# Kernel optimization log

Hardware: AMD Instinct MI355X
Metric: run time of the kernel (lower is better)

The kernel has to match this reference:

```python
import jax, jax.numpy as jnp
import numpy as np

NUM_CLASSES = 8      # cls-head channels per anchor; channel 0 = background
A = 3                # anchors per location (aspect ratios 0.5, 1.0, 2.0)
K = 500              # fixed pre-NMS top-k per (image, class, level)
SCORE_TH = 0.05
IOU_TH = 0.5
# (H, W, stride, anchor_size) per FPN level for a 1536x1536 image
LEVELS = ((192, 192, 8, 16.0), (96, 96, 16, 32.0), (48, 48, 32, 64.0))
ARS = np.array([0.5, 1.0, 2.0], dtype=np.float32)


def make_anchors(H, W, stride, size):
    w = size * np.sqrt(ARS)           # (A,)
    h = size / np.sqrt(ARS)
    cx = (np.arange(W, dtype=np.float32) + 0.5) * stride
    cy = (np.arange(H, dtype=np.float32) + 0.5) * stride
    cy, cx = np.meshgrid(cy, cx, indexing='ij')   # (H, W)
    x1 = cx[..., None] - 0.5 * w
    y1 = cy[..., None] - 0.5 * h
    x2 = cx[..., None] + 0.5 * w
    y2 = cy[..., None] + 0.5 * h
    return jnp.asarray(np.stack([x1, y1, x2, y2], -1).reshape(-1, 4))  # (H*W*A, 4)


def decode(anchors, deltas):
    # anchors (N,4) xyxy, deltas (B,N,4) -> boxes (B,N,4); matches source decode math
    wa = anchors[:, 2] - anchors[:, 0]
    ha = anchors[:, 3] - anchors[:, 1]
    cxa = anchors[:, 0] + 0.5 * wa
    cya = anchors[:, 1] + 0.5 * ha
    dx, dy, dw, dh = deltas[..., 0], deltas[..., 1], deltas[..., 2], deltas[..., 3]
    cx = dx * wa + cxa
    cy = dy * ha + cya
    w = jnp.exp(dw) * wa
    h = jnp.exp(dh) * ha
    return jnp.stack([cx - 0.5 * w, cy - 0.5 * h, cx + 0.5 * w, cy + 0.5 * h], -1)


def nms_one(boxes, scores):
    # boxes (N,4), scores (N,) for one (image, class). Fixed-shape exact greedy NMS
    # over the top-K candidates (boxes below SCORE_TH are invalidated, matching the
    # source's mask; K bounds the candidate set for jit-compatibility).
    sc, idx = jax.lax.top_k(scores, K)
    b = boxes[idx]                                        # (K,4) sorted by score desc
    valid = sc > SCORE_TH
    area = (b[:, 2] - b[:, 0]) * (b[:, 3] - b[:, 1])
    ix1 = jnp.maximum(b[:, None, 0], b[None, :, 0])
    iy1 = jnp.maximum(b[:, None, 1], b[None, :, 1])
    ix2 = jnp.minimum(b[:, None, 2], b[None, :, 2])
    iy2 = jnp.minimum(b[:, None, 3], b[None, :, 3])
    inter = jnp.maximum(ix2 - ix1, 0.0) * jnp.maximum(iy2 - iy1, 0.0)
    union = area[:, None] + area[None, :] - inter
    iou = inter / jnp.maximum(union, 1e-9)                # (K,K)
    r = jnp.arange(K)

    def body(i, keep):
        sup = (iou[i] > IOU_TH) & (r > i) & keep[i]
        return keep & ~sup

    keep = jax.lax.fori_loop(0, K, body, valid)
    return b, sc, keep


def level_postprocess(cls_p, reg_p, anchors):
    B = cls_p.shape[0]
    # (B, A*C, H, W) -> sigmoid scores (B, N, C); (B, A*4, H, W) -> deltas (B, N, 4)
    scores = jax.nn.sigmoid(cls_p.transpose(0, 2, 3, 1).reshape(B, -1, NUM_CLASSES))
    deltas = reg_p.transpose(0, 2, 3, 1).reshape(B, -1, 4)
    boxes = decode(anchors, deltas)                       # (B, N, 4)
    fg = scores[:, :, 1:]                                 # foreground classes 1..C-1

    def per_image(b_i, s_i):                              # b_i (N,4), s_i (N, C-1)
        return jax.vmap(lambda s: nms_one(b_i, s))(s_i.T)

    return jax.vmap(per_image)(boxes, fg)                 # each (B, C-1, K, ...)


def setup_inputs() -> dict:
    key = jax.random.key(0)
    ks = jax.random.split(key, 6)
    B = 16
    inp = {}
    for i, (H, W, _, _) in enumerate(LEVELS):
        # cls logits shifted by -4 ~ RetinaNet prior bias so only a sparse subset
        # passes the 0.05 threshold; reg deltas small-scale like trained outputs.
        inp[f'cls_p{i + 3}'] = jax.random.normal(ks[i], (B, A * NUM_CLASSES, H, W), jnp.float32) - 4.0
        inp[f'reg_p{i + 3}'] = jax.random.normal(ks[i + 3], (B, A * 4, H, W), jnp.float32) * 0.1
    return inp


def reference(cls_p3, cls_p4, cls_p5, reg_p3, reg_p4, reg_p5):
    cls_ps = (cls_p3, cls_p4, cls_p5)
    reg_ps = (reg_p3, reg_p4, reg_p5)
    boxes_l, scores_l, keep_l = [], [], []
    for cls_p, reg_p, (H, W, stride, size) in zip(cls_ps, reg_ps, LEVELS):
        anchors = make_anchors(H, W, stride, size)
        b, s, k = level_postprocess(cls_p, reg_p, anchors)
        boxes_l.append(b)
        scores_l.append(s)
        keep_l.append(k)
    boxes = jnp.stack(boxes_l)      # (3, B, C-1, K, 4)
    scores = jnp.stack(scores_l)    # (3, B, C-1, K)
    keep = jnp.stack(keep_l)        # (3, B, C-1, K) bool
    B = cls_p3.shape[0]
    labels = jnp.broadcast_to(jnp.arange(NUM_CLASSES - 1)[None, None, :, None],
                              (3, B, NUM_CLASSES - 1, K))
    return boxes, scores, keep, labels
```

## Files before the change

kernel.cpp:

```cpp
#include <hip/hip_runtime.h>
#include <stdint.h>


namespace {
constexpr int KSEL = 500;
constexpr int CAP  = 1024;
constexpr int BIMG = 16;
constexpr int NCLS = 7;
constexpr int NPROB = 336;
constexpr int OFF_SCORES = 672000;
constexpr int OFF_KEEP   = 840000;
constexpr int OFF_LABELS = 1008000;

constexpr unsigned KEY_F0 = 2051;
constexpr unsigned KEY_F1 = 2045;
constexpr unsigned KEY_F2 = 2039;

constexpr unsigned SB15 = (0x3D000000u >> 15);
constexpr int NB15 = 2048;

constexpr int NB_SCAN = 1232;
constexpr int SEG0 = 384;
constexpr int SEG1 = 1024;
constexpr int SEG2 = 1536;
constexpr size_t L1_POOL_BASE = (size_t)896 * SEG0;
constexpr size_t L2_POOL_BASE = L1_POOL_BASE + (size_t)224 * SEG1;
constexpr size_t POOL_ENTRIES = L2_POOL_BASE + (size_t)112 * SEG2;

constexpr size_t CCNT_OFF   = 0;
constexpr size_t CHIST_OFF  = 8192;
constexpr size_t CHIST_BYTES = (size_t)NB_SCAN * NB15 * 4;
constexpr size_t POOL_OFF   = CHIST_OFF + CHIST_BYTES;
constexpr size_t POOL_BYTES = POOL_ENTRIES * 8;
constexpr size_t WS_NEED    = POOL_OFF + POOL_BYTES;

__constant__ unsigned char c_tb[36] = {
    0,0,0,0,0,0,0,0, 1,1,1,1,1,1,1, 2,2,2,2,2,2,
    3,3,3,3,3, 4,4,4,4, 5,5,5, 6,6, 7};
__constant__ unsigned char c_tw[36] = {
    0,1,2,3,4,5,6,7, 1,2,3,4,5,6,7, 2,3,4,5,6,7,
    3,4,5,6,7, 4,5,6,7, 5,6,7, 6,7, 7};

typedef float f4v __attribute__((ext_vector_type(4)));
}

__device__ __forceinline__ float sigmoid_ref(float x) {
#pragma clang fp contract(off)
    return 1.0f / (1.0f + expf(-x));
}

__device__ __forceinline__ unsigned mono_key(float x) {
    unsigned b = __float_as_uint(x);
    unsigned m = (b & 0x80000000u) ? 0xFFFFFFFFu : 0x80000000u;
    return b ^ m;
}

__device__ __forceinline__ void scan_decode(int bx, int& l, int& img, int& c,
                                            int& p, int& HW, int& hw0, int& hw1) {
    int pidL, chunk, chunkHW;
    if (bx < 896)        { l = 0; pidL = bx >> 3;         chunk = bx & 7;         chunkHW = 4608; HW = 36864; }
    else if (bx < 1120)  { l = 1; pidL = (bx - 896) >> 1; chunk = (bx - 896) & 1; chunkHW = 4608; HW = 9216; }
    else                 { l = 2; pidL = bx - 1120;       chunk = 0;              chunkHW = 2304; HW = 2304; }
    img = pidL / NCLS; c = pidL % NCLS;
    p = (l * BIMG + img) * NCLS + c;
    hw0 = chunk * chunkHW; hw1 = hw0 + chunkHW;
}

__global__ __launch_bounds__(256) void k_scan(
    const float* __restrict__ cls0, const float* __restrict__ cls1,
    const float* __restrict__ cls2, unsigned* __restrict__ g_ccnt,
    unsigned long long* __restrict__ g_pool, unsigned* __restrict__ g_chist)
{
    const int tid = threadIdx.x;
    int l, img, c, p, HW, hw0, hw1;
    scan_decode(blockIdx.x, l, img, c, p, HW, hw0, hw1);
    (void)p;
    const float* cls = (l == 0) ? cls0 : (l == 1) ? cls1 : cls2;
    const unsigned keyf = (l == 0) ? KEY_F0 : (l == 1) ? KEY_F1 : KEY_F2;
    const int segCap = (l == 0) ? SEG0 : (l == 1) ? SEG1 : SEG2;
    size_t segOff;
    if (l == 0)      segOff = (size_t)blockIdx.x * SEG0;
    else if (l == 1) segOff = L1_POOL_BASE + (size_t)(blockIdx.x - 896) * SEG1;
    else             segOff = L2_POOL_BASE + (size_t)(blockIdx.x - 1120) * SEG2;

    __shared__ unsigned long long buf[SEG2];
    __shared__ unsigned lh[NB15];
    __shared__ int s_n;
    for (int i = tid; i < NB15; i += 256) lh[i] = 0u;
    if (tid == 0) s_n = 0;
    __syncthreads();

    const int n4 = (hw1 - hw0) >> 2;
    for (int a = 0; a < 3; ++a) {
        const f4v* pb4 = (const f4v*)(cls
            + (size_t)(img * 24 + a * 8 + c + 1) * (size_t)HW + (size_t)hw0);
        for (int idx = tid; idx < n4; idx += 256) {
            f4v v = __builtin_nontemporal_load(pb4 + idx);
            float mx = fmaxf(fmaxf(v.x, v.y), fmaxf(v.z, v.w));
            if ((mono_key(mx) >> 19) < keyf) continue;
            const int hwb = hw0 + idx * 4;
            float vv[4] = {v.x, v.y, v.z, v.w};
#pragma unroll
            for (int q = 0; q < 4; ++q) {
                if ((mono_key(vv[q]) >> 19) >= keyf) {
                    int pos = atomicAdd(&s_n, 1);
                    unsigned bits = __float_as_uint(sigmoid_ref(vv[q]));
                    unsigned bin = (bits >> 15) - SB15;
                    if (bin > (unsigned)(NB15 - 1)) bin = NB15 - 1;
                    atomicAdd(&lh[bin], 1u);
                    if (pos < segCap) {
                        unsigned n = (unsigned)((hwb + q) * 3 + a);
                        buf[pos] = ((unsigned long long)bits << 32)
                                 | (unsigned long long)(0xFFFFFFFFu - n);
                    }
                }
            }
        }
    }
    __syncthreads();
    int m = s_n; if (m > segCap) m = segCap;
    unsigned long long* seg = g_pool + segOff;
    for (int i = tid; i < m; i += 256) seg[i] = buf[i];
    unsigned* ch = g_chist + (size_t)blockIdx.x * NB15;
    for (int i = tid; i < NB15; i += 256) ch[i] = lh[i];
    if (tid == 0) g_ccnt[blockIdx.x] = (unsigned)m;
}

__global__ __launch_bounds__(512) void k_nms2(
    const float* __restrict__ reg0, const float* __restrict__ reg1,
    const float* __restrict__ reg2, const unsigned* __restrict__ g_ccnt,
    const unsigned long long* __restrict__ g_pool,
    const unsigned* __restrict__ g_chist, float* __restrict__ out)
{
    const int p    = blockIdx.x;
    const int l    = p / (BIMG * NCLS);
    const int rem  = p % (BIMG * NCLS);
    const int bimg = rem / NCLS;
    const int c    = rem % NCLS;
    const int tid  = threadIdx.x;
    const int lane = tid & 63;
    const int wid  = tid >> 6;

    int W, HW; float stride, asize;
    const float* reg;
    int nseg, segEnt, ccntBase;
    size_t segOff0;
    if (l == 0)      { W = 192; HW = 36864; stride = 8.0f;  asize = 16.0f; reg = reg0;
                       nseg = 8; segEnt = SEG0; ccntBase = rem * 8;
                       segOff0 = (size_t)rem * 8 * SEG0; }
    else if (l == 1) { W = 96;  HW = 9216;  stride = 16.0f; asize = 32.0f; reg = reg1;
                       nseg = 2; segEnt = SEG1; ccntBase = 896 + rem * 2;
                       segOff0 = L1_POOL_BASE + (size_t)rem * 2 * SEG1; }
    else             { W = 48;  HW = 2304;  stride = 32.0f; asize = 64.0f; reg = reg2;
                       nseg = 1; segEnt = SEG2; ccntBase = 1120 + rem;
                       segOff0 = L2_POOL_BASE + (size_t)rem * SEG2; }

    __shared__ union {
        struct { unsigned h[NB15]; unsigned s4[512]; } a;
        struct { float4 box4[512]; float sarea[512]; } b;
    } u;
    __shared__ unsigned sup[64];
    __shared__ unsigned s_t;
    __shared__ int      s_n;
    __shared__ unsigned long long s_keys[CAP];
    __shared__ unsigned long long s_sorted[CAP];
    __shared__ unsigned long long s_mask[8][512];
    __shared__ unsigned long long s_alive[8];

    for (int i = tid; i < NB15; i += 512) {
        unsigned acc = 0;
        for (int s = 0; s < nseg; ++s)
            acc += g_chist[(size_t)(ccntBase + s) * NB15 + i];
        u.a.h[i] = acc;
    }
    for (int i = tid; i < CAP; i += 512) s_sorted[i] = 0ull;
    if (tid == 0) { s_t = 0u; s_n = 0; }
    __syncthreads();

    {
        unsigned cs = u.a.h[tid * 4] + u.a.h[tid * 4 + 1]
                    + u.a.h[tid * 4 + 2] + u.a.h[tid * 4 + 3];
        u.a.s4[tid] = cs;
    }
    __syncthreads();
    if (tid < 64) {
        unsigned ss = 0;
#pragma unroll
        for (int k = 0; k < 8; ++k) ss += u.a.s4[tid * 8 + k];
        sup[tid] = ss;
    }
    __syncthreads();
    if (tid < 64) {
        unsigned Sab = 0;
        for (int j = tid + 1; j < 64; ++j) Sab += sup[j];
        if (Sab < (unsigned)KSEL && Sab + sup[tid] >= (unsigned)KSEL) {
            unsigned acc = Sab;
            int t = tid * 32;
            for (int b = tid * 32 + 31; b >= tid * 32; --b) {
                acc += u.a.h[b];
                if (acc >= (unsigned)KSEL) { t = b; break; }
            }
            s_t = (unsigned)t;
        }
    }
    __syncthreads();

    const unsigned t  = s_t;
    const unsigned tg = (t > 0u) ? (t - 1u) : 0u;
    const unsigned cut = (tg + SB15) << 15;

    for (int s = 0; s < nseg; ++s) {
        const unsigned long long* seg = g_pool + segOff0 + (size_t)s * segEnt;
        unsigned cn = g_ccnt[ccntBase + s]; if (cn > (unsigned)segEnt) cn = segEnt;
        for (int i = tid; i < (int)cn; i += 512) {
            unsigned long long key = seg[i];
            if ((unsigned)(key >> 32) >= cut) {
                int pos = atomicAdd(&s_n, 1);
                if (pos < CAP) s_keys[pos] = key;
            }
        }
    }
    __syncthreads();
    const int mm = (s_n > CAP) ? CAP : s_n;

    for (int i = tid; i < mm; i += 512) {
        const unsigned long long ki = s_keys[i];
        int rank = 0;
        for (int j = 0; j < mm; ++j) rank += (int)(s_keys[j] > ki);
        if (rank < CAP) s_sorted[rank] = ki;
    }
    __syncthreads();

    float4* outBoxes4 = (float4*)(out + (size_t)p * (size_t)(KSEL * 4));
    float* outScores = out + OFF_SCORES + (size_t)p * KSEL;
    float* outLabels = out + OFF_LABELS + (size_t)p * KSEL;

    {
        const int r = tid;
        bool pred = false;
        if (r < KSEL) {
            unsigned long long key = s_sorted[r];
            unsigned bits = (unsigned)(key >> 32);
            float sc = __uint_as_float(bits);
            unsigned n = 0xFFFFFFFFu - (unsigned)(key & 0xFFFFFFFFull);
            int a  = (int)(n % 3u);
            int hw = (int)(n / 3u);
            int h2 = hw / W, w = hw % W;
            float b0, b1, b2, b3;
            {
#pragma clang fp contract(off)
                float ar  = (a == 0) ? 0.5f : ((a == 1) ? 1.0f : 2.0f);
                float sq  = sqrtf(ar);
                float was = asize * sq;
                float has = asize / sq;
                float cx0 = ((float)w + 0.5f) * stride;
                float cy0 = ((float)h2 + 0.5f) * stride;
                float x1 = cx0 - 0.5f * was;
                float y1 = cy0 - 0.5f * has;
                float x2 = cx0 + 0.5f * was;
                float y2 = cy0 + 0.5f * has;
                float wa = x2 - x1;
                float ha = y2 - y1;
                float cxa = x1 + 0.5f * wa;
                float cya = y1 + 0.5f * ha;
                const float* rp = reg + (size_t)(bimg * 12 + a * 4) * (size_t)HW + (size_t)hw;
                float dx = rp[0];
                float dy = rp[(size_t)HW];
                float dw = rp[(size_t)2 * HW];
                float dh = rp[(size_t)3 * HW];
                float bcx = dx * wa + cxa;
                float bcy = dy * ha + cya;
                float bw  = expf(dw) * wa;
                float bh  = expf(dh) * ha;
                b0 = bcx - 0.5f * bw;
                b1 = bcy - 0.5f * bh;
                b2 = bcx + 0.5f * bw;
                b3 = bcy + 0.5f * bh;
                u.b.box4[r]  = make_float4(b0, b1, b2, b3);
                u.b.sarea[r] = (b2 - b0) * (b3 - b1);
            }
            outBoxes4[r] = make_float4(b0, b1, b2, b3);
            outScores[r] = sc;
            outLabels[r] = (float)c;
            pred = sc > 0.05f;
        }
        unsigned long long bal = __ballot((int)pred);
        if (lane == 0) s_alive[wid] = bal;
    }
    __syncthreads();

    for (int t2 = wid; t2 < 36; t2 += 8) {
        const int b = (int)c_tb[t2];
        const int w = (int)c_tw[t2];
        const int r2 = b * 64 + lane;
        const float4 rb = u.b.box4[r2];
        const float  A0 = u.b.sarea[r2];
        const int jn = (w * 64 + 64 <= KSEL) ? 64 : (KSEL - w * 64);
        const unsigned long long full =
            (jn == 64) ? ~0ull : ((1ull << jn) - 1ull);

        unsigned long long m = 0ull;
#pragma unroll
        for (int k = 0; k < 64; ++k) {
#pragma clang fp contract(off)
            float4 cb = u.b.box4[w * 64 + k];
            float  ja = u.b.sarea[w * 64 + k];
            float ix1 = fmaxf(rb.x, cb.x);
            float iy1 = fmaxf(rb.y, cb.y);
            float ix2 = fminf(rb.z, cb.z);
            float iy2 = fminf(rb.w, cb.w);
            float iw = fmaxf(ix2 - ix1, 0.0f);
            float ih = fmaxf(iy2 - iy1, 0.0f);
            float inter = iw * ih;
            float uni = A0 + ja - inter;
            float uc  = fmaxf(uni, 1e-9f);
            if (inter + inter > uc) m |= (1ull << k);
        }
        m &= full;
        if (b == w) m &= ~(1ull << lane);

        s_mask[w][r2] = m;
    }
    __syncthreads();

    if (wid == 0) {
        unsigned long long alive[8];
#pragma unroll
        for (int w = 0; w < 8; ++w) alive[w] = s_alive[w];

#pragma unroll
        for (int b = 0; b < 8; ++b) {
            unsigned long long a64 = alive[b];
            if (!a64) continue;
            const unsigned long long diag = s_mask[b][b * 64 + lane];
            const unsigned long long hiL =
                (lane < 63) ? (~0ull << (lane + 1)) : 0ull;

            unsigned long long work = a64, removed = 0ull;
            while (true) {
                bool active = (((work >> lane) & 1ull) != 0ull) &&
                              ((diag & work & hiL) != 0ull);
                unsigned long long act = __ballot((int)active);
                if (!act) break;
                int j = __ffsll((long long)act) - 1;
                unsigned long long wj = __ballot((int)((diag >> j) & 1ull));
                unsigned long long hij = (j < 63) ? (~0ull << (j + 1)) : 0ull;
                wj &= hij;
                removed |= wj;
                work &= hij;
                work &= ~wj;
            }
            const unsigned long long kept = a64 & ~removed;
            alive[b] = kept;

            if (b < 7 && kept) {
                const bool iskept = ((kept >> lane) & 1ull) != 0ull;
#pragma unroll
                for (int w = b + 1; w < 8; ++w) {
                    unsigned long long v = s_mask[w][b * 64 + lane];
                    unsigned long long contrib = iskept ? v : 0ull;
                    if (!__any((int)(contrib != 0ull))) continue;
#pragma unroll
                    for (int s = 32; s >= 1; s >>= 1)
                        contrib |= __shfl_xor(contrib, s);
                    alive[w] &= ~contrib;
                }
            }
        }

        float* outKeep = out + OFF_KEEP + (size_t)p * KSEL;
#pragma unroll
        for (int it = 0; it < 8; ++it) {
            int r = it * 64 + lane;
            if (r < KSEL)
                outKeep[r] = ((alive[r >> 6] >> (r & 63)) & 1ull) ? 1.0f : 0.0f;
        }
    }
}

__global__ __launch_bounds__(256) void retina_post_kernel(
    const float* __restrict__ cls0, const float* __restrict__ reg0,
    const float* __restrict__ cls1, const float* __restrict__ reg1,
    const float* __restrict__ cls2, const float* __restrict__ reg2,
    float* __restrict__ out)
{
    const int bx   = blockIdx.x;
    const int l    = bx / (BIMG * NCLS);
    const int rem  = bx % (BIMG * NCLS);
    const int bimg = rem / NCLS;
    const int c    = rem % NCLS;
    const int tid  = threadIdx.x;
    const int lane = tid & 63;
    const int wid  = tid >> 6;

    int H, W; float stride, asize;
    const float *cls, *reg;
    if (l == 0)      { H = 192; W = 192; stride = 8.0f;  asize = 16.0f; cls = cls0; reg = reg0; }
    else if (l == 1) { H = 96;  W = 96;  stride = 16.0f; asize = 32.0f; cls = cls1; reg = reg1; }
    else             { H = 48;  W = 48;  stride = 32.0f; asize = 64.0f; cls = cls2; reg = reg2; }
    const int HW = H * W;
    const int c1 = c + 1;

    __shared__ unsigned long long s_keys[CAP];
    __shared__ float              s_box[KSEL * 4];
    __shared__ float              s_area[KSEL];
    __shared__ unsigned long long s_mask[KSEL * 8];
    __shared__ unsigned long long s_alive[8];
    __shared__ unsigned           s_hist[4 * 16];
    __shared__ unsigned           s_prefix;
    __shared__ unsigned           s_cgt;
    __shared__ int                s_m;
    __shared__ int                s_need4;
    __shared__ int                s_gshift;

    for (int i = tid; i < CAP; i += 256) s_keys[i] = 0ull;
    if (tid == 0) { s_prefix = 0u; s_cgt = 0u; s_m = 0; s_need4 = 0; s_gshift = 20; }

    for (int pass = 0; pass < 4; ++pass) {
        if (pass == 3 && !s_need4) break;
        if (tid < 64) s_hist[tid] = 0u;
        __syncthreads();
        const unsigned pref = s_prefix;
        const unsigned cgt  = s_cgt;
        const int shp = 32 - 4 * pass;
        const int shn = 28 - 4 * pass;
        unsigned cnt[16];
#pragma unroll
        for (int q = 0; q < 16; ++q) cnt[q] = 0u;
        for (int a = 0; a < 3; ++a) {
            const float* p = cls + (size_t)(bimg * 24 + a * 8 + c1) * (size_t)HW;
            for (int hw = tid; hw < HW; hw += 256) {
                float s = sigmoid_ref(p[hw]);
                unsigned bits = __float_as_uint(s);
                bool match = (pass == 0) || ((bits >> shp) == pref);
                unsigned sel = match ? ((bits >> shn) & 0xFu) : 0xFFu;
#pragma unroll
                for (int q = 0; q < 16; ++q) {
                    unsigned long long bal = __ballot((int)(sel == (unsigned)q));
                    cnt[q] += (unsigned)__popcll(bal);
                }
            }
        }
        if (lane == 0) {
#pragma unroll
            for (int q = 0; q < 16; ++q) s_hist[wid * 16 + q] = cnt[q];
        }
        __syncthreads();
        if (tid == 0) {
            unsigned tot[16];
#pragma unroll
            for (int q = 0; q < 16; ++q)
                tot[q] = s_hist[q] + s_hist[16 + q] + s_hist[32 + q] + s_hist[48 + q];
            unsigned acc = cgt;
            int t = 0;
            for (int q = 15; q >= 0; --q) {
                if (acc + tot[q] >= (unsigned)KSEL) { t = q; break; }
                acc += tot[q];
            }
            s_prefix = (pref << 4) | (unsigned)t;
            s_cgt = acc;
            if (pass == 2) s_need4 = (acc + tot[t] > (unsigned)CAP) ? 1 : 0;
            if (pass == 3) s_gshift = 16;
        }
        __syncthreads();
    }

    {
        const unsigned gpref = s_prefix;
        const int gsh = s_gshift;
        for (int a = 0; a < 3; ++a) {
            const float* p = cls + (size_t)(bimg * 24 + a * 8 + c1) * (size_t)HW;
            for (int hw = tid; hw < HW; hw += 256) {
                float s = sigmoid_ref(p[hw]);
                unsigned bits = __float_as_uint(s);
                if ((bits >> gsh) >= gpref) {
                    int pos = atomicAdd(&s_m, 1);
                    if (pos < CAP) {
                        unsigned n = (unsigned)(hw * 3 + a);
                        s_keys[pos] = ((unsigned long long)bits << 32)
                                    | (unsigned long long)(0xFFFFFFFFu - n);
                    }
                }
            }
        }
    }

    for (int k2 = 2; k2 <= CAP; k2 <<= 1) {
        for (int j = k2 >> 1; j >= 1; j >>= 1) {
            __syncthreads();
            for (int i = tid; i < CAP; i += 256) {
                int ixj = i ^ j;
                if (ixj > i) {
                    unsigned long long va = s_keys[i], vb = s_keys[ixj];
                    bool desc = ((i & k2) == 0);
                    if (desc ? (va < vb) : (va > vb)) {
                        s_keys[i] = vb; s_keys[ixj] = va;
                    }
                }
            }
        }
    }
    __syncthreads();

    const size_t probIdx  = (size_t)((l * BIMG + bimg) * NCLS + c);
    float* outBoxes  = out + probIdx * (size_t)(KSEL * 4);
    float* outScores = out + OFF_SCORES + probIdx * (size_t)KSEL;
    float* outKeep   = out + OFF_KEEP   + probIdx * (size_t)KSEL;
    float* outLabels = out + OFF_LABELS + probIdx * (size_t)KSEL;

    for (int it = 0; it < 2; ++it) {
        int r = it * 256 + tid;
        bool pred = false;
        if (r < KSEL) {
            unsigned long long key = s_keys[r];
            unsigned bits = (unsigned)(key >> 32);
            float sc = __uint_as_float(bits);
            unsigned n = 0xFFFFFFFFu - (unsigned)(key & 0xFFFFFFFFull);
            int a  = (int)(n % 3u);
            int hw = (int)(n / 3u);
            int h = hw / W, w = hw % W;
            float b0, b1, b2, b3;
            {
#pragma clang fp contract(off)
                float ar  = (a == 0) ? 0.5f : ((a == 1) ? 1.0f : 2.0f);
                float sq  = sqrtf(ar);
                float was = asize * sq;
                float has = asize / sq;
                float cx0 = ((float)w + 0.5f) * stride;
                float cy0 = ((float)h + 0.5f) * stride;
                float x1 = cx0 - 0.5f * was;
                float y1 = cy0 - 0.5f * has;
                float x2 = cx0 + 0.5f * was;
                float y2 = cy0 + 0.5f * has;
                float wa = x2 - x1;
                float ha = y2 - y1;
                float cxa = x1 + 0.5f * wa;
                float cya = y1 + 0.5f * ha;
                const float* rp = reg + (size_t)(bimg * 12 + a * 4) * (size_t)HW + (size_t)hw;
                float dx = rp[0];
                float dy = rp[(size_t)HW];
                float dw = rp[(size_t)2 * HW];
                float dh = rp[(size_t)3 * HW];
                float bcx = dx * wa + cxa;
                float bcy = dy * ha + cya;
                float bw  = expf(dw) * wa;
                float bh  = expf(dh) * ha;
                b0 = bcx - 0.5f * bw;
                b1 = bcy - 0.5f * bh;
                b2 = bcx + 0.5f * bw;
                b3 = bcy + 0.5f * bh;
                s_box[r * 4 + 0] = b0; s_box[r * 4 + 1] = b1;
                s_box[r * 4 + 2] = b2; s_box[r * 4 + 3] = b3;
                s_area[r] = (b2 - b0) * (b3 - b1);
            }
            outBoxes[r * 4 + 0] = b0; outBoxes[r * 4 + 1] = b1;
            outBoxes[r * 4 + 2] = b2; outBoxes[r * 4 + 3] = b3;
            outScores[r] = sc;
            outLabels[r] = (float)c;
            pred = sc > 0.05f;
        }
        unsigned long long bal = __ballot((int)pred);
        if (lane == 0) s_alive[it * 4 + wid] = bal;
    }
    __syncthreads();

    for (int i = tid; i < KSEL; i += 256) {
        float x1i = s_box[i * 4 + 0], y1i = s_box[i * 4 + 1];
        float x2i = s_box[i * 4 + 2], y2i = s_box[i * 4 + 3];
        float ai = s_area[i];
        for (int ww = 0; ww < 8; ++ww) {
            unsigned long long m = 0ull;
            int jbase = ww * 64;
            int jend = jbase + 64; if (jend > KSEL) jend = KSEL;
            int j0 = jbase > (i + 1) ? jbase : (i + 1);
            for (int j = j0; j < jend; ++j) {
#pragma clang fp contract(off)
                float ix1 = fmaxf(x1i, s_box[j * 4 + 0]);
                float iy1 = fmaxf(y1i, s_box[j * 4 + 1]);
                float ix2 = fminf(x2i, s_box[j * 4 + 2]);
                float iy2 = fminf(y2i, s_box[j * 4 + 3]);
                float iw = fmaxf(ix2 - ix1, 0.0f);
                float ih = fmaxf(iy2 - iy1, 0.0f);
                float inter = iw * ih;
                float uni = ai + s_area[j] - inter;
                float iou = inter / fmaxf(uni, 1e-9f);
                if (iou > 0.5f) m |= (1ull << (j - jbase));
            }
            s_mask[i * 8 + ww] = m;
        }
    }
    __syncthreads();

    if (tid < 64) {
        unsigned long long al = (lane < 8) ? s_alive[lane] : 0ull;
        for (int i = 0; i < KSEL; ++i) {
            unsigned long long aw = __shfl(al, i >> 6);
            if ((aw >> (i & 63)) & 1ull) {
                if (lane < 8) al &= ~s_mask[i * 8 + lane];
            }
        }
        if (lane < 8) s_alive[lane] = al;
    }
    __syncthreads();

    for (int it = 0; it < 2; ++it) {
        int r = it * 256 + tid;
        if (r < KSEL) {
            unsigned long long w64 = s_alive[r >> 6];
            outKeep[r] = ((w64 >> (r & 63)) & 1ull) ? 1.0f : 0.0f;
        }
    }
}

extern "C" void kernel_launch(void* const* d_in, const int* in_sizes, int n_in,
                              void* d_out, int out_size, void* d_ws, size_t ws_size,
                              hipStream_t stream) {
    (void)out_size;
    const float *cls0 = nullptr, *reg0 = nullptr, *cls1 = nullptr,
                *reg1 = nullptr, *cls2 = nullptr, *reg2 = nullptr;
    for (int i = 0; i < n_in; ++i) {
        switch (in_sizes[i]) {
            case 14155776: cls0 = (const float*)d_in[i]; break;
            case 7077888:  reg0 = (const float*)d_in[i]; break;
            case 3538944:  cls1 = (const float*)d_in[i]; break;
            case 1769472:  reg1 = (const float*)d_in[i]; break;
            case 884736:   cls2 = (const float*)d_in[i]; break;
            case 442368:   reg2 = (const float*)d_in[i]; break;
            default: break;
        }
    }
    float* out = (float*)d_out;

    if (ws_size < WS_NEED) {
        retina_post_kernel<<<dim3(NPROB), dim3(256), 0, stream>>>(
            cls0, reg0, cls1, reg1, cls2, reg2, out);
        return;
    }

    unsigned*           g_ccnt  = (unsigned*)((char*)d_ws + CCNT_OFF);
    unsigned*           g_chist = (unsigned*)((char*)d_ws + CHIST_OFF);
    unsigned long long* g_pool  = (unsigned long long*)((char*)d_ws + POOL_OFF);

    k_scan<<<dim3(NB_SCAN), dim3(256), 0, stream>>>(cls0, cls1, cls2,
                                                    g_ccnt, g_pool, g_chist);
    k_nms2<<<dim3(NPROB), dim3(512), 0, stream>>>(reg0, reg1, reg2,
                                                  g_ccnt, g_pool, g_chist,
                                                  out);
}
```

Measured before the change: 209.0 us.

## Coarsen score histogram, fuse rank sort with box decode, readlane IoU operands

The score histogram shrinks from 2048 to 512 bins, so each NMS block accumulates and scans fewer bins and the scan kernel writes less histogram data to global memory. The separate rank-sort pass into s_sorted is removed: each thread computes its candidate's rank, issues the regression loads before the rank loop so their latency overlaps it, then writes the decoded box directly at its rank and sets alive bits with shared atomicOr. The IoU mask loop now broadcasts column boxes with readlane instead of reading them from LDS at each step. Coarser bins may pass more candidates above the cutoff, which can make the O(n^2) rank count costlier, and boxes at ranks the candidates do not fill are no longer explicitly zeroed.

```diff
diff --git a/kernel.cpp b/kernel.cpp
--- a/kernel.cpp
+++ b/kernel.cpp
@@ -16,8 +16,8 @@
 constexpr unsigned KEY_F1 = 2045;
 constexpr unsigned KEY_F2 = 2039;
 
-constexpr unsigned SB15 = (0x3D000000u >> 15);
-constexpr int NB15 = 2048;
+constexpr unsigned SBH = (0x3D000000u >> 17);
+constexpr int NBH = 512;
 
 constexpr int NB_SCAN = 1232;
 constexpr int SEG0 = 384;
@@ -29,7 +29,7 @@
 
 constexpr size_t CCNT_OFF   = 0;
 constexpr size_t CHIST_OFF  = 8192;
-constexpr size_t CHIST_BYTES = (size_t)NB_SCAN * NB15 * 4;
+constexpr size_t CHIST_BYTES = (size_t)NB_SCAN * NBH * 4;
 constexpr size_t POOL_OFF   = CHIST_OFF + CHIST_BYTES;
 constexpr size_t POOL_BYTES = POOL_ENTRIES * 8;
 constexpr size_t WS_NEED    = POOL_OFF + POOL_BYTES;
@@ -53,6 +53,10 @@
     unsigned b = __float_as_uint(x);
     unsigned m = (b & 0x80000000u) ? 0xFFFFFFFFu : 0x80000000u;
     return b ^ m;
+}
+
+__device__ __forceinline__ float rl(float v, int k) {
+    return __uint_as_float(__builtin_amdgcn_readlane(__float_as_uint(v), k));
 }
 
 __device__ __forceinline__ void scan_decode(int bx, int& l, int& img, int& c,
@@ -84,9 +88,9 @@
     else             segOff = L2_POOL_BASE + (size_t)(blockIdx.x - 1120) * SEG2;
 
     __shared__ unsigned long long buf[SEG2];
-    __shared__ unsigned lh[NB15];
+    __shared__ unsigned lh[NBH];
     __shared__ int s_n;
-    for (int i = tid; i < NB15; i += 256) lh[i] = 0u;
+    for (int i = tid; i < NBH; i += 256) lh[i] = 0u;
     if (tid == 0) s_n = 0;
     __syncthreads();
 
@@ -105,8 +109,8 @@
                 if ((mono_key(vv[q]) >> 19) >= keyf) {
                     int pos = atomicAdd(&s_n, 1);
                     unsigned bits = __float_as_uint(sigmoid_ref(vv[q]));
-                    unsigned bin = (bits >> 15) - SB15;
-                    if (bin > (unsigned)(NB15 - 1)) bin = NB15 - 1;
+                    unsigned bin = (bits >> 17) - SBH;
+                    if (bin > (unsigned)(NBH - 1)) bin = NBH - 1;
                     atomicAdd(&lh[bin], 1u);
                     if (pos < segCap) {
                         unsigned n = (unsigned)((hwb + q) * 3 + a);
@@ -121,8 +125,8 @@
     int m = s_n; if (m > segCap) m = segCap;
     unsigned long long* seg = g_pool + segOff;
     for (int i = tid; i < m; i += 256) seg[i] = buf[i];
-    unsigned* ch = g_chist + (size_t)blockIdx.x * NB15;
-    for (int i = tid; i < NB15; i += 256) ch[i] = lh[i];
+    unsigned* ch = g_chist + (size_t)blockIdx.x * NBH;
+    for (int i = tid; i < NBH; i += 256) ch[i] = lh[i];
     if (tid == 0) g_ccnt[blockIdx.x] = (unsigned)m;
 }
 
@@ -156,37 +160,30 @@
                        segOff0 = L2_POOL_BASE + (size_t)rem * SEG2; }
 
     __shared__ union {
-        struct { unsigned h[NB15]; unsigned s4[512]; } a;
+        struct { unsigned h[NBH]; } a;
         struct { float4 box4[512]; float sarea[512]; } b;
     } u;
     __shared__ unsigned sup[64];
     __shared__ unsigned s_t;
     __shared__ int      s_n;
     __shared__ unsigned long long s_keys[CAP];
-    __shared__ unsigned long long s_sorted[CAP];
     __shared__ unsigned long long s_mask[8][512];
     __shared__ unsigned long long s_alive[8];
 
-    for (int i = tid; i < NB15; i += 512) {
+    {
         unsigned acc = 0;
         for (int s = 0; s < nseg; ++s)
-            acc += g_chist[(size_t)(ccntBase + s) * NB15 + i];
-        u.a.h[i] = acc;
-    }
-    for (int i = tid; i < CAP; i += 512) s_sorted[i] = 0ull;
+            acc += g_chist[(size_t)(ccntBase + s) * NBH + tid];
+        u.a.h[tid] = acc;
+    }
+    if (tid < 8) s_alive[tid] = 0ull;
     if (tid == 0) { s_t = 0u; s_n = 0; }
     __syncthreads();
 
-    {
-        unsigned cs = u.a.h[tid * 4] + u.a.h[tid * 4 + 1]
-                    + u.a.h[tid * 4 + 2] + u.a.h[tid * 4 + 3];
-        u.a.s4[tid] = cs;
-    }
-    __syncthreads();
     if (tid < 64) {
         unsigned ss = 0;
 #pragma unroll
-        for (int k = 0; k < 8; ++k) ss += u.a.s4[tid * 8 + k];
+        for (int k = 0; k < 8; ++k) ss += u.a.h[tid * 8 + k];
         sup[tid] = ss;
     }
     __syncthreads();
@@ -195,8 +192,8 @@
         for (int j = tid + 1; j < 64; ++j) Sab += sup[j];
         if (Sab < (unsigned)KSEL && Sab + sup[tid] >= (unsigned)KSEL) {
             unsigned acc = Sab;
-            int t = tid * 32;
-            for (int b = tid * 32 + 31; b >= tid * 32; --b) {
+            int t = tid * 8;
+            for (int b = tid * 8 + 7; b >= tid * 8; --b) {
                 acc += u.a.h[b];
                 if (acc >= (unsigned)KSEL) { t = b; break; }
             }
@@ -207,7 +204,7 @@
 
     const unsigned t  = s_t;
     const unsigned tg = (t > 0u) ? (t - 1u) : 0u;
-    const unsigned cut = (tg + SB15) << 15;
+    const unsigned cut = (tg + SBH) << 17;
 
     for (int s = 0; s < nseg; ++s) {
         const unsigned long long* seg = g_pool + segOff0 + (size_t)s * segEnt;
@@ -223,69 +220,65 @@
     __syncthreads();
     const int mm = (s_n > CAP) ? CAP : s_n;
 
-    for (int i = tid; i < mm; i += 512) {
-        const unsigned long long ki = s_keys[i];
-        int rank = 0;
-        for (int j = 0; j < mm; ++j) rank += (int)(s_keys[j] > ki);
-        if (rank < CAP) s_sorted[rank] = ki;
-    }
-    __syncthreads();
-
     float4* outBoxes4 = (float4*)(out + (size_t)p * (size_t)(KSEL * 4));
     float* outScores = out + OFF_SCORES + (size_t)p * KSEL;
     float* outLabels = out + OFF_LABELS + (size_t)p * KSEL;
 
-    {
-        const int r = tid;
-        bool pred = false;
-        if (r < KSEL) {
-            unsigned long long key = s_sorted[r];
-            unsigned bits = (unsigned)(key >> 32);
-            float sc = __uint_as_float(bits);
-            unsigned n = 0xFFFFFFFFu - (unsigned)(key & 0xFFFFFFFFull);
-            int a  = (int)(n % 3u);
-            int hw = (int)(n / 3u);
-            int h2 = hw / W, w = hw % W;
-            float b0, b1, b2, b3;
-            {
+    for (int base = 0; base < CAP; base += 512) {
+        const int i = base + tid;
+        if (i < mm) {
+            const unsigned long long ki = s_keys[i];
+            const unsigned bits = (unsigned)(ki >> 32);
+            const unsigned n = 0xFFFFFFFFu - (unsigned)(ki & 0xFFFFFFFFull);
+            const int a  = (int)(n % 3u);
+            const int hw = (int)(n / 3u);
+            const float* rp = reg + (size_t)(bimg * 12 + a * 4) * (size_t)HW + (size_t)hw;
+            const float dx = rp[0];
+            const float dy = rp[(size_t)HW];
+            const float dw = rp[(size_t)2 * HW];
+            const float dh = rp[(size_t)3 * HW];
+
+            int rank = 0;
+            for (int j = 0; j < mm; ++j) rank += (int)(s_keys[j] > ki);
+
+            if (rank < KSEL) {
+                const float sc = __uint_as_float(bits);
+                const int h2 = hw / W, w = hw % W;
+                float b0, b1, b2, b3;
+                {
 #pragma clang fp contract(off)
-                float ar  = (a == 0) ? 0.5f : ((a == 1) ? 1.0f : 2.0f);
-                float sq  = sqrtf(ar);
-                float was = asize * sq;
-                float has = asize / sq;
-                float cx0 = ((float)w + 0.5f) * stride;
-                float cy0 = ((float)h2 + 0.5f) * stride;
-                float x1 = cx0 - 0.5f * was;
-                float y1 = cy0 - 0.5f * has;
-                float x2 = cx0 + 0.5f * was;
-                float y2 = cy0 + 0.5f * has;
-                float wa = x2 - x1;
-                float ha = y2 - y1;
-                float cxa = x1 + 0.5f * wa;
-                float cya = y1 + 0.5f * ha;
-                const float* rp = reg + (size_t)(bimg * 12 + a * 4) * (size_t)HW + (size_t)hw;
-                float dx = rp[0];
-                float dy = rp[(size_t)HW];
-                float dw = rp[(size_t)2 * HW];
-                float dh = rp[(size_t)3 * HW];
-                float bcx = dx * wa + cxa;
-                float bcy = dy * ha + cya;
-                float bw  = expf(dw) * wa;
-                float bh  = expf(dh) * ha;
-                b0 = bcx - 0.5f * bw;
-                b1 = bcy - 0.5f * bh;
-                b2 = bcx + 0.5f * bw;
-                b3 = bcy + 0.5f * bh;
-                u.b.box4[r]  = make_float4(b0, b1, b2, b3);
-                u.b.sarea[r] = (b2 - b0) * (b3 - b1);
-            }
-            outBoxes4[r] = make_float4(b0, b1, b2, b3);
-            outScores[r] = sc;
-            outLabels[r] = (float)c;
-            pred = sc > 0.05f;
-        }
-        unsigned long long bal = __ballot((int)pred);
-        if (lane == 0) s_alive[wid] = bal;
+                    float ar  = (a == 0) ? 0.5f : ((a == 1) ? 1.0f : 2.0f);
+                    float sq  = sqrtf(ar);
+                    float was = asize * sq;
+                    float has = asize / sq;
+                    float cx0 = ((float)w + 0.5f) * stride;
+                    float cy0 = ((float)h2 + 0.5f) * stride;
+                    float x1 = cx0 - 0.5f * was;
+                    float y1 = cy0 - 0.5f * has;
+                    float x2 = cx0 + 0.5f * was;
+                    float y2 = cy0 + 0.5f * has;
+                    float wa = x2 - x1;
+                    float ha = y2 - y1;
+                    float cxa = x1 + 0.5f * wa;
+                    float cya = y1 + 0.5f * ha;
+                    float bcx = dx * wa + cxa;
+                    float bcy = dy * ha + cya;
+                    float bw  = expf(dw) * wa;
+                    float bh  = expf(dh) * ha;
+                    b0 = bcx - 0.5f * bw;
+                    b1 = bcy - 0.5f * bh;
+                    b2 = bcx + 0.5f * bw;
+                    b3 = bcy + 0.5f * bh;
+                    u.b.box4[rank]  = make_float4(b0, b1, b2, b3);
+                    u.b.sarea[rank] = (b2 - b0) * (b3 - b1);
+                }
+                outBoxes4[rank] = make_float4(b0, b1, b2, b3);
+                outScores[rank] = sc;
+                outLabels[rank] = (float)c;
+                if (sc > 0.05f)
+                    atomicOr(&s_alive[rank >> 6], 1ull << (rank & 63));
+            }
+        }
     }
     __syncthreads();
 
@@ -295,6 +288,8 @@
         const int r2 = b * 64 + lane;
         const float4 rb = u.b.box4[r2];
         const float  A0 = u.b.sarea[r2];
+        const float4 cbl = u.b.box4[w * 64 + lane];
+        const float  cal = u.b.sarea[w * 64 + lane];
         const int jn = (w * 64 + 64 <= KSEL) ? 64 : (KSEL - w * 64);
         const unsigned long long full =
             (jn == 64) ? ~0ull : ((1ull << jn) - 1ull);
@@ -303,12 +298,15 @@
 #pragma unroll
         for (int k = 0; k < 64; ++k) {
 #pragma clang fp contract(off)
-            float4 cb = u.b.box4[w * 64 + k];
-            float  ja = u.b.sarea[w * 64 + k];
-            float ix1 = fmaxf(rb.x, cb.x);
-            float iy1 = fmaxf(rb.y, cb.y);
-            float ix2 = fminf(rb.z, cb.z);
-            float iy2 = fminf(rb.w, cb.w);
+            float jx1 = rl(cbl.x, k);
+            float jy1 = rl(cbl.y, k);
+            float jx2 = rl(cbl.z, k);
+            float jy2 = rl(cbl.w, k);
+            float ja  = rl(cal, k);
+            float ix1 = fmaxf(rb.x, jx1);
+            float iy1 = fmaxf(rb.y, jy1);
+            float ix2 = fminf(rb.z, jx2);
+            float iy2 = fminf(rb.w, jy2);
             float iw = fmaxf(ix2 - ix1, 0.0f);
             float ih = fmaxf(iy2 - iy1, 0.0f);
             float inter = iw * ih;
```

Measured after the change: 218.7 us. 1.05x slower.
